# Kernel tuning notes

Measured on AMD Instinct MI355X. Metric: run time of the kernel, lower is better.

Reference implementation:

```python
import jax, jax.numpy as jnp
import numpy as np

EPS = 1e-12
B, S, H, NH = 4, 2048, 512, 8
DH = H // NH

def layernorm(x, g, b):
    mu = jnp.mean(x, axis=-1, keepdims=True)
    var = jnp.mean((x - mu) ** 2, axis=-1, keepdims=True)
    return (x - mu) * jax.lax.rsqrt(var + EPS) * g + b

def setup_inputs() -> dict:
    key = jax.random.key(0)
    ks = jax.random.split(key, 12)
    s = 0.02
    return {
        "hidden_states": jax.random.normal(ks[0], (B, S, H), dtype=jnp.float32),
        "attention_mask": jnp.zeros((B, 1, 1, S), dtype=jnp.float32),
        "ln1_g": jnp.ones((H,), jnp.float32), "ln1_b": jnp.zeros((H,), jnp.float32),
        "wq": jax.random.normal(ks[1], (H, H), jnp.float32) * s, "bq": jnp.zeros((H,), jnp.float32),
        "wk": jax.random.normal(ks[2], (H, H), jnp.float32) * s, "bk": jnp.zeros((H,), jnp.float32),
        "wv": jax.random.normal(ks[3], (H, H), jnp.float32) * s, "bv": jnp.zeros((H,), jnp.float32),
        "wo": jax.random.normal(ks[4], (H, H), jnp.float32) * s, "bo": jnp.zeros((H,), jnp.float32),
        "ln2_g": jnp.ones((H,), jnp.float32), "ln2_b": jnp.zeros((H,), jnp.float32),
    }

def _heads(x):  # [B,S,H] -> [B,NH,S,DH]
    return x.reshape(B, S, NH, DH).transpose(0, 2, 1, 3)

def reference(hidden_states, attention_mask, ln1_g, ln1_b, wq, bq, wk, bk, wv, bv, wo, bo, ln2_g, ln2_b):
    h = layernorm(hidden_states, ln1_g, ln1_b)  # Pre-LN
    q = _heads(h @ wq.T + bq)
    k = _heads(h @ wk.T + bk)
    v = _heads(h @ wv.T + bv)
    scores = jnp.einsum("bhqd,bhkd->bhqk", q, k) / jnp.sqrt(jnp.float32(DH))
    scores = scores + attention_mask  # additive BERT mask
    probs = jax.nn.softmax(scores, axis=-1)
    ctx = jnp.einsum("bhqk,bhkd->bhqd", probs, v)
    ctx = ctx.transpose(0, 2, 1, 3).reshape(B, S, H)
    # BertSelfOutput: LN(dense(ctx) + residual), residual is the LN'd hidden per module code
    out = layernorm(ctx @ wo.T + bo + h, ln2_g, ln2_b)
    return out
```

## Files before the change

kernel.cpp:

```cpp
#include <hip/hip_runtime.h>

typedef __bf16 bf16;
typedef __bf16 bf16x2 __attribute__((ext_vector_type(2)));
typedef __bf16 bf16x4 __attribute__((ext_vector_type(4)));
typedef __bf16 bf16x8 __attribute__((ext_vector_type(8)));
typedef float f32x4 __attribute__((ext_vector_type(4)));

typedef __attribute__((address_space(1))) const void g_void;
typedef __attribute__((address_space(3))) void l_void;

constexpr int Bsz = 4, S = 2048, H = 512, NH = 8, DH = 64;
constexpr int M = Bsz * S;
constexpr int K = H;
constexpr int WELEM = H * H;
constexpr float LOG2E  = 1.44269504f;
constexpr float QSCALE = 0.125f * LOG2E;

__global__ __launch_bounds__(256) void convert_w(
    const float* __restrict__ w0, const float* __restrict__ w1,
    const float* __restrict__ w2, const float* __restrict__ w3,
    bf16* __restrict__ dst) {
    int y = blockIdx.y;
    const float* src = (y == 0) ? w0 : (y == 1) ? w1 : (y == 2) ? w2 : w3;
    bf16* d = dst + (size_t)y * WELEM;
    int i = (blockIdx.x * 256 + threadIdx.x) * 4;
    float4 v = *(const float4*)(src + i);
    bf16x4 o;
    o.x = (bf16)v.x; o.y = (bf16)v.y; o.z = (bf16)v.z; o.w = (bf16)v.w;
    *(bf16x4*)(d + i) = o;
}

__global__ __launch_bounds__(256) void scale_mask(
    const float* __restrict__ m, float* __restrict__ out) {
    int i = blockIdx.x * 256 + threadIdx.x;
    out[i] = m[i] * LOG2E;
}

__global__ __launch_bounds__(256) void ln_f32_bf16(
    const float* __restrict__ x, const float* __restrict__ g,
    const float* __restrict__ b, bf16* __restrict__ y) {
    int row = blockIdx.x;
    int t = threadIdx.x;
    float2 xv = *(const float2*)(x + (size_t)row * H + t * 2);
    float v0 = xv.x, v1 = xv.y;
    float s = v0 + v1, s2 = v0 * v0 + v1 * v1;
    for (int off = 1; off < 64; off <<= 1) {
        s  += __shfl_xor(s,  off, 64);
        s2 += __shfl_xor(s2, off, 64);
    }
    __shared__ float red[8];
    int wid = t >> 6;
    if ((t & 63) == 0) { red[wid * 2] = s; red[wid * 2 + 1] = s2; }
    __syncthreads();
    s  = red[0] + red[2] + red[4] + red[6];
    s2 = red[1] + red[3] + red[5] + red[7];
    float mu  = s * (1.0f / H);
    float var = s2 * (1.0f / H) - mu * mu;
    float inv = rsqrtf(var + 1e-12f);
    float2 gv = *(const float2*)(g + t * 2);
    float2 bv = *(const float2*)(b + t * 2);
    bf16x2 out;
    out.x = (bf16)((v0 - mu) * inv * gv.x + bv.x);
    out.y = (bf16)((v1 - mu) * inv * gv.y + bv.y);
    *(bf16x2*)(y + (size_t)row * H + t * 2) = out;
}

__global__ __launch_bounds__(256) void ln_bf16_f32(
    const bf16* __restrict__ x, const float* __restrict__ g,
    const float* __restrict__ b, float* __restrict__ y) {
    int row = blockIdx.x;
    int t = threadIdx.x;
    bf16x2 xv = *(const bf16x2*)(x + (size_t)row * H + t * 2);
    float v0 = (float)xv.x, v1 = (float)xv.y;
    float s = v0 + v1, s2 = v0 * v0 + v1 * v1;
    for (int off = 1; off < 64; off <<= 1) {
        s  += __shfl_xor(s,  off, 64);
        s2 += __shfl_xor(s2, off, 64);
    }
    __shared__ float red[8];
    int wid = t >> 6;
    if ((t & 63) == 0) { red[wid * 2] = s; red[wid * 2 + 1] = s2; }
    __syncthreads();
    s  = red[0] + red[2] + red[4] + red[6];
    s2 = red[1] + red[3] + red[5] + red[7];
    float mu  = s * (1.0f / H);
    float var = s2 * (1.0f / H) - mu * mu;
    float inv = rsqrtf(var + 1e-12f);
    float2 gv = *(const float2*)(g + t * 2);
    float2 bv = *(const float2*)(b + t * 2);
    float2 out;
    out.x = (v0 - mu) * inv * gv.x + bv.x;
    out.y = (v1 - mu) * inv * gv.y + bv.y;
    *(float2*)(y + (size_t)row * H + t * 2) = out;
}

__device__ inline void gemm128_mainloop(const bf16* __restrict__ A,
                                        const bf16* __restrict__ W,
                                        int bm, int bn,
                                        bf16* As, bf16* Bs, f32x4 acc[4][4]) {
    int t = threadIdx.x;
    int lane = t & 63, wid = t >> 6;
    int quad = lane >> 4, n = lane & 15;
    int wm = wid & 1, wn = wid >> 1;
    int sw = (n & 7) * 8;
    int srow = lane >> 3;
    int scol = (lane & 7) * 8;
    for (int kt = 0; kt < K; kt += 64) {
        __syncthreads();
        #pragma unroll
        for (int i = 0; i < 4; i++) {
            int chunk = wid * 4 + i;
            int row = chunk * 8 + srow;
            int csrc = scol ^ ((row & 7) * 8);
            __builtin_amdgcn_global_load_lds(
                (g_void*)&A[(size_t)(bm + row) * K + kt + csrc],
                (l_void*)&As[chunk * 512], 16, 0, 0);
            __builtin_amdgcn_global_load_lds(
                (g_void*)&W[(size_t)(bn + row) * K + kt + csrc],
                (l_void*)&Bs[chunk * 512], 16, 0, 0);
        }
        __syncthreads();
        #pragma unroll
        for (int half = 0; half < 2; half++) {
            bf16x8 af[4], bf[4];
            #pragma unroll
            for (int mi = 0; mi < 4; mi++) {
                int c = (half * 32 + quad * 8) ^ sw;
                af[mi] = *(const bf16x8*)&As[(wm * 64 + mi * 16 + n) * 64 + c];
                bf[mi] = *(const bf16x8*)&Bs[(wn * 64 + mi * 16 + n) * 64 + c];
            }
            #pragma unroll
            for (int mi = 0; mi < 4; mi++)
                #pragma unroll
                for (int ni = 0; ni < 4; ni++)
                    acc[mi][ni] = __builtin_amdgcn_mfma_f32_16x16x32_bf16(
                        af[mi], bf[ni], acc[mi][ni], 0, 0, 0);
        }
    }
}

__global__ __launch_bounds__(256) void gemm_qkv(
    const bf16* __restrict__ h, const bf16* __restrict__ wb,
    const float* __restrict__ bq, const float* __restrict__ bk,
    const float* __restrict__ bv,
    bf16* __restrict__ qd, bf16* __restrict__ kd, bf16* __restrict__ vtd) {
    __shared__ alignas(16) bf16 As[128 * 64];
    __shared__ alignas(16) bf16 Bs[128 * 64];
    int bm = blockIdx.x * 128, bn = blockIdx.y * 128, z = blockIdx.z;
    const bf16* W = wb + (size_t)z * WELEM;
    const float* bias = (z == 0) ? bq : (z == 1) ? bk : bv;
    f32x4 acc[4][4];
    for (int mi = 0; mi < 4; mi++)
        for (int ni = 0; ni < 4; ni++)
            for (int r = 0; r < 4; r++) acc[mi][ni][r] = 0.0f;
    gemm128_mainloop(h, W, bm, bn, As, Bs, acc);
    int lane = threadIdx.x & 63, wid = threadIdx.x >> 6;
    int quad = lane >> 4, n = lane & 15;
    int wm = wid & 1, wn = wid >> 1;
    for (int mi = 0; mi < 4; mi++)
        for (int ni = 0; ni < 4; ni++)
            for (int r = 0; r < 4; r++) {
                int i = bm + wm * 64 + mi * 16 + quad * 4 + r;
                int j = bn + wn * 64 + ni * 16 + n;
                float val = acc[mi][ni][r] + bias[j];
                if (z == 0) val *= QSCALE;
                int b = i >> 11, srow = i & (S - 1);
                int nh = j >> 6, d = j & (DH - 1);
                if (z < 2) {
                    bf16* dst = (z == 0) ? qd : kd;
                    dst[(((size_t)(b * NH + nh)) * S + srow) * DH + d] = (bf16)val;
                } else {
                    vtd[(((size_t)(b * NH + nh)) * DH + d) * S + srow] = (bf16)val;
                }
            }
}

__global__ __launch_bounds__(256) void gemm_out(
    const bf16* __restrict__ ctx, const bf16* __restrict__ wo,
    const float* __restrict__ bo, const bf16* __restrict__ resid,
    bf16* __restrict__ dst) {
    __shared__ alignas(16) bf16 As[128 * 64];
    __shared__ alignas(16) bf16 Bs[128 * 64];
    int bm = blockIdx.x * 128, bn = blockIdx.y * 128;
    f32x4 acc[4][4];
    for (int mi = 0; mi < 4; mi++)
        for (int ni = 0; ni < 4; ni++)
            for (int r = 0; r < 4; r++) acc[mi][ni][r] = 0.0f;
    gemm128_mainloop(ctx, wo, bm, bn, As, Bs, acc);
    int lane = threadIdx.x & 63, wid = threadIdx.x >> 6;
    int quad = lane >> 4, n = lane & 15;
    int wm = wid & 1, wn = wid >> 1;
    for (int mi = 0; mi < 4; mi++)
        for (int ni = 0; ni < 4; ni++)
            for (int r = 0; r < 4; r++) {
                int i = bm + wm * 64 + mi * 16 + quad * 4 + r;
                int j = bn + wn * 64 + ni * 16 + n;
                float val = acc[mi][ni][r] + bo[j]
                          + (float)resid[(size_t)i * H + j];
                dst[(size_t)i * H + j] = (bf16)val;
            }
}

constexpr int LDP9 = 72;

#if __has_builtin(__builtin_amdgcn_exp2f)
#define EXP2(x) __builtin_amdgcn_exp2f(x)
#else
#define EXP2(x) exp2f(x)
#endif

__global__ __launch_bounds__(512, 4) void attn_kernel(
    const bf16* __restrict__ q, const bf16* __restrict__ k,
    const bf16* __restrict__ vt, const float* __restrict__ mask2,
    bf16* __restrict__ ctx) {
    int bh = blockIdx.y;
    int b = bh >> 3, nh = bh & 7;
    int t = threadIdx.x, wid = t >> 6, lane = t & 63;
    int quad = lane >> 4, n = lane & 15;
    int qg = wid >> 1, kh = wid & 1;
    int qbase = blockIdx.x * 128 + qg * 32;
    int kO = kh * 64;

    const bf16* Qp = q  + (size_t)bh * S * DH;
    const bf16* Kp = k  + (size_t)bh * S * DH;
    const bf16* Vt = vt + (size_t)bh * DH * S;
    const float* mrow = mask2 + (size_t)b * S;

    __shared__ alignas(16) bf16 smem[34816];
    bf16* Ks = smem;
    bf16* Vs = smem + 8192;
    bf16* Pw = smem + 16384 + wid * (32 * LDP9);

    int sw = (n & 7) * 8;

    bf16x8 qf[2][2];
    #pragma unroll
    for (int qt = 0; qt < 2; qt++)
        #pragma unroll
        for (int hh = 0; hh < 2; hh++)
            qf[qt][hh] = *(const bf16x8*)
                &Qp[(size_t)(qbase + qt * 16 + n) * DH + hh * 32 + quad * 8];

    f32x4 O[2][4];
    #pragma unroll
    for (int qt = 0; qt < 2; qt++)
        for (int i = 0; i < 4; i++)
            for (int r = 0; r < 4; r++) O[qt][i][r] = 0.0f;
    float l_run[2] = {0.0f, 0.0f};

    for (int kb = 0; kb < S; kb += 128) {
        __syncthreads();
        #pragma unroll
        for (int i = 0; i < 2; i++) {
            int c = t + i * 512;
            {
                int row = c >> 3, part = c & 7;
                int csrc = (part * 8) ^ ((row & 7) * 8);
                __builtin_amdgcn_global_load_lds(
                    (g_void*)&Kp[(size_t)(kb + row) * DH + csrc],
                    (l_void*)&Ks[c * 8], 16, 0, 0);
            }
            {
                int row = c >> 4, part = c & 15;
                int csrc = (part * 8) ^ ((row & 7) * 8);
                __builtin_amdgcn_global_load_lds(
                    (g_void*)&Vt[(size_t)row * S + kb + csrc],
                    (l_void*)&Vs[c * 8], 16, 0, 0);
            }
        }
        __syncthreads();

        #pragma unroll
        for (int kt = 0; kt < 4; kt++) {
            const bf16* kr = &Ks[(kO + kt * 16 + n) * 64];
            bf16x8 ka = *(const bf16x8*)&kr[(quad * 8) ^ sw];
            bf16x8 kc = *(const bf16x8*)&kr[(32 + quad * 8) ^ sw];
            float4 mk = *(const float4*)&mrow[kb + kO + kt * 16 + quad * 4];
            #pragma unroll
            for (int qt = 0; qt < 2; qt++) {
                f32x4 s;
                for (int r = 0; r < 4; r++) s[r] = 0.0f;
                s = __builtin_amdgcn_mfma_f32_16x16x32_bf16(ka, qf[qt][0], s, 0, 0, 0);
                s = __builtin_amdgcn_mfma_f32_16x16x32_bf16(kc, qf[qt][1], s, 0, 0, 0);
                float p0 = EXP2(s[0] + mk.x);
                float p1 = EXP2(s[1] + mk.y);
                float p2 = EXP2(s[2] + mk.z);
                float p3 = EXP2(s[3] + mk.w);
                l_run[qt] += (p0 + p1) + (p2 + p3);
                bf16x4 w;
                w[0] = (bf16)p0; w[1] = (bf16)p1; w[2] = (bf16)p2; w[3] = (bf16)p3;
                *(bf16x4*)&Pw[(qt * 16 + n) * LDP9 + kt * 16 + quad * 4] = w;
            }
        }

        __builtin_amdgcn_s_setprio(1);
        #pragma unroll
        for (int ks = 0; ks < 2; ks++)
            #pragma unroll
            for (int qt = 0; qt < 2; qt++) {
                bf16x8 pf = *(const bf16x8*)
                    &Pw[(qt * 16 + n) * LDP9 + ks * 32 + quad * 8];
                #pragma unroll
                for (int dt = 0; dt < 4; dt++) {
                    bf16x8 vf = *(const bf16x8*)
                        &Vs[(dt * 16 + n) * 128 + ((kO + ks * 32 + quad * 8) ^ sw)];
                    O[qt][dt] = __builtin_amdgcn_mfma_f32_16x16x32_bf16(
                        vf, pf, O[qt][dt], 0, 0, 0);
                }
            }
        __builtin_amdgcn_s_setprio(0);
    }

    float* Ob = (float*)smem;
    float* Lb = Ob + 4 * 32 * 68;
    __syncthreads();
    if (kh) {
        #pragma unroll
        for (int qt = 0; qt < 2; qt++) {
            #pragma unroll
            for (int dt = 0; dt < 4; dt++)
                *(f32x4*)&Ob[(qg * 32 + qt * 16 + n) * 68 + dt * 16 + quad * 4]
                    = O[qt][dt];
            Lb[(qg * 2 + qt) * 64 + lane] = l_run[qt];
        }
    }
    __syncthreads();
    if (!kh) {
        #pragma unroll
        for (int qt = 0; qt < 2; qt++) {
            float l = l_run[qt] + Lb[(qg * 2 + qt) * 64 + lane];
            l += __shfl_xor(l, 16, 64);
            l += __shfl_xor(l, 32, 64);
            float linv = 1.0f / l;
            int srow = qbase + qt * 16 + n;
            #pragma unroll
            for (int dt = 0; dt < 4; dt++) {
                f32x4 po = *(const f32x4*)
                    &Ob[(qg * 32 + qt * 16 + n) * 68 + dt * 16 + quad * 4];
                bf16x4 o4;
                for (int r = 0; r < 4; r++)
                    o4[r] = (bf16)((O[qt][dt][r] + po[r]) * linv);
                int col = nh * 64 + dt * 16 + quad * 4;
                *(bf16x4*)&ctx[((size_t)(b * S + srow)) * H + col] = o4;
            }
        }
    }
}

extern "C" void kernel_launch(void* const* d_in, const int* in_sizes, int n_in,
                              void* d_out, int out_size, void* d_ws, size_t ws_size,
                              hipStream_t stream) {
    const float* hidden = (const float*)d_in[0];
    const float* mask   = (const float*)d_in[1];
    const float* ln1_g  = (const float*)d_in[2];
    const float* ln1_b  = (const float*)d_in[3];
    const float* wq = (const float*)d_in[4],  *bq = (const float*)d_in[5];
    const float* wk = (const float*)d_in[6],  *bk = (const float*)d_in[7];
    const float* wv = (const float*)d_in[8],  *bv = (const float*)d_in[9];
    const float* wo = (const float*)d_in[10], *bo = (const float*)d_in[11];
    const float* ln2_g = (const float*)d_in[12];
    const float* ln2_b = (const float*)d_in[13];

    const size_t T = (size_t)M * H;
    bf16* wb  = (bf16*)d_ws;
    bf16* h   = wb  + (size_t)4 * WELEM;
    bf16* qd  = h   + T;
    bf16* kd  = qd  + T;
    bf16* vtd = kd  + T;
    bf16* ctx = vtd + T;
    float* mask2 = (float*)(ctx + T);
    bf16* tmp = qd;

    convert_w<<<dim3(WELEM / 1024, 4), 256, 0, stream>>>(wq, wk, wv, wo, wb);
    scale_mask<<<Bsz * S / 256, 256, 0, stream>>>(mask, mask2);
    ln_f32_bf16<<<M, 256, 0, stream>>>(hidden, ln1_g, ln1_b, h);
    gemm_qkv<<<dim3(M / 128, H / 128, 3), 256, 0, stream>>>(
        h, wb, bq, bk, bv, qd, kd, vtd);
    attn_kernel<<<dim3(S / 128, Bsz * NH), 512, 0, stream>>>(qd, kd, vtd, mask2, ctx);
    gemm_out<<<dim3(M / 128, H / 128), 256, 0, stream>>>(
        ctx, wb + (size_t)3 * WELEM, bo, h, tmp);
    ln_bf16_f32<<<M, 256, 0, stream>>>(tmp, ln2_g, ln2_b, (float*)d_out);
}
```

Baseline: 202.1 us.

## Fuse prep kernels and stage V-transpose through shared memory for coalesced stores

Merges the weight conversion, mask scaling and first LayerNorm into a single launch, with block ranges selecting the task, so two kernel launches go away. In the QKV GEMM, the V-transpose epilogue now writes the tile into padded shared memory and then stores 16-byte vectors along the sequence dimension, replacing the scattered 2-byte strided global writes. This costs an extra shared-memory buffer and two barriers in the V blocks.

```diff
diff --git a/kernel.cpp b/kernel.cpp
--- a/kernel.cpp
+++ b/kernel.cpp
@@ -16,53 +16,53 @@
 constexpr float LOG2E  = 1.44269504f;
 constexpr float QSCALE = 0.125f * LOG2E;
 
-__global__ __launch_bounds__(256) void convert_w(
+__global__ __launch_bounds__(256) void prep(
+    const float* __restrict__ hidden, const float* __restrict__ ln1_g,
+    const float* __restrict__ ln1_b,
     const float* __restrict__ w0, const float* __restrict__ w1,
     const float* __restrict__ w2, const float* __restrict__ w3,
-    bf16* __restrict__ dst) {
-    int y = blockIdx.y;
-    const float* src = (y == 0) ? w0 : (y == 1) ? w1 : (y == 2) ? w2 : w3;
-    bf16* d = dst + (size_t)y * WELEM;
-    int i = (blockIdx.x * 256 + threadIdx.x) * 4;
-    float4 v = *(const float4*)(src + i);
-    bf16x4 o;
-    o.x = (bf16)v.x; o.y = (bf16)v.y; o.z = (bf16)v.z; o.w = (bf16)v.w;
-    *(bf16x4*)(d + i) = o;
-}
-
-__global__ __launch_bounds__(256) void scale_mask(
-    const float* __restrict__ m, float* __restrict__ out) {
-    int i = blockIdx.x * 256 + threadIdx.x;
-    out[i] = m[i] * LOG2E;
-}
-
-__global__ __launch_bounds__(256) void ln_f32_bf16(
-    const float* __restrict__ x, const float* __restrict__ g,
-    const float* __restrict__ b, bf16* __restrict__ y) {
-    int row = blockIdx.x;
+    const float* __restrict__ mask,
+    bf16* __restrict__ h, bf16* __restrict__ wb, float* __restrict__ mask2) {
+    int bx = blockIdx.x;
     int t = threadIdx.x;
-    float2 xv = *(const float2*)(x + (size_t)row * H + t * 2);
-    float v0 = xv.x, v1 = xv.y;
-    float s = v0 + v1, s2 = v0 * v0 + v1 * v1;
-    for (int off = 1; off < 64; off <<= 1) {
-        s  += __shfl_xor(s,  off, 64);
-        s2 += __shfl_xor(s2, off, 64);
-    }
-    __shared__ float red[8];
-    int wid = t >> 6;
-    if ((t & 63) == 0) { red[wid * 2] = s; red[wid * 2 + 1] = s2; }
-    __syncthreads();
-    s  = red[0] + red[2] + red[4] + red[6];
-    s2 = red[1] + red[3] + red[5] + red[7];
-    float mu  = s * (1.0f / H);
-    float var = s2 * (1.0f / H) - mu * mu;
-    float inv = rsqrtf(var + 1e-12f);
-    float2 gv = *(const float2*)(g + t * 2);
-    float2 bv = *(const float2*)(b + t * 2);
-    bf16x2 out;
-    out.x = (bf16)((v0 - mu) * inv * gv.x + bv.x);
-    out.y = (bf16)((v1 - mu) * inv * gv.y + bv.y);
-    *(bf16x2*)(y + (size_t)row * H + t * 2) = out;
+    if (bx < M) {
+        int row = bx;
+        float2 xv = *(const float2*)(hidden + (size_t)row * H + t * 2);
+        float v0 = xv.x, v1 = xv.y;
+        float s = v0 + v1, s2 = v0 * v0 + v1 * v1;
+        for (int off = 1; off < 64; off <<= 1) {
+            s  += __shfl_xor(s,  off, 64);
+            s2 += __shfl_xor(s2, off, 64);
+        }
+        __shared__ float red[8];
+        int wid = t >> 6;
+        if ((t & 63) == 0) { red[wid * 2] = s; red[wid * 2 + 1] = s2; }
+        __syncthreads();
+        s  = red[0] + red[2] + red[4] + red[6];
+        s2 = red[1] + red[3] + red[5] + red[7];
+        float mu  = s * (1.0f / H);
+        float var = s2 * (1.0f / H) - mu * mu;
+        float inv = rsqrtf(var + 1e-12f);
+        float2 gv = *(const float2*)(ln1_g + t * 2);
+        float2 bv = *(const float2*)(ln1_b + t * 2);
+        bf16x2 out;
+        out.x = (bf16)((v0 - mu) * inv * gv.x + bv.x);
+        out.y = (bf16)((v1 - mu) * inv * gv.y + bv.y);
+        *(bf16x2*)(h + (size_t)row * H + t * 2) = out;
+    } else if (bx < M + 1024) {
+        int idx = bx - M;
+        int y = idx >> 8, xx = idx & 255;
+        const float* src = (y == 0) ? w0 : (y == 1) ? w1 : (y == 2) ? w2 : w3;
+        bf16* d = wb + (size_t)y * WELEM;
+        int i = (xx * 256 + t) * 4;
+        float4 v = *(const float4*)(src + i);
+        bf16x4 o;
+        o.x = (bf16)v.x; o.y = (bf16)v.y; o.z = (bf16)v.z; o.w = (bf16)v.w;
+        *(bf16x4*)(d + i) = o;
+    } else {
+        int i = (bx - M - 1024) * 256 + t;
+        mask2[i] = mask[i] * LOG2E;
+    }
 }
 
 __global__ __launch_bounds__(256) void ln_bf16_f32(
@@ -144,8 +144,9 @@
     const float* __restrict__ bq, const float* __restrict__ bk,
     const float* __restrict__ bv,
     bf16* __restrict__ qd, bf16* __restrict__ kd, bf16* __restrict__ vtd) {
-    __shared__ alignas(16) bf16 As[128 * 64];
-    __shared__ alignas(16) bf16 Bs[128 * 64];
+    __shared__ alignas(16) bf16 smem[17408];
+    bf16* As = smem;
+    bf16* Bs = smem + 8192;
     int bm = blockIdx.x * 128, bn = blockIdx.y * 128, z = blockIdx.z;
     const bf16* W = wb + (size_t)z * WELEM;
     const float* bias = (z == 0) ? bq : (z == 1) ? bk : bv;
@@ -154,25 +155,47 @@
         for (int ni = 0; ni < 4; ni++)
             for (int r = 0; r < 4; r++) acc[mi][ni][r] = 0.0f;
     gemm128_mainloop(h, W, bm, bn, As, Bs, acc);
-    int lane = threadIdx.x & 63, wid = threadIdx.x >> 6;
+    int t = threadIdx.x;
+    int lane = t & 63, wid = t >> 6;
     int quad = lane >> 4, n = lane & 15;
     int wm = wid & 1, wn = wid >> 1;
-    for (int mi = 0; mi < 4; mi++)
-        for (int ni = 0; ni < 4; ni++)
-            for (int r = 0; r < 4; r++) {
-                int i = bm + wm * 64 + mi * 16 + quad * 4 + r;
-                int j = bn + wn * 64 + ni * 16 + n;
-                float val = acc[mi][ni][r] + bias[j];
-                if (z == 0) val *= QSCALE;
-                int b = i >> 11, srow = i & (S - 1);
-                int nh = j >> 6, d = j & (DH - 1);
-                if (z < 2) {
-                    bf16* dst = (z == 0) ? qd : kd;
+    if (z < 2) {
+        bf16* dst = (z == 0) ? qd : kd;
+        for (int mi = 0; mi < 4; mi++)
+            for (int ni = 0; ni < 4; ni++)
+                for (int r = 0; r < 4; r++) {
+                    int i = bm + wm * 64 + mi * 16 + quad * 4 + r;
+                    int j = bn + wn * 64 + ni * 16 + n;
+                    float val = acc[mi][ni][r] + bias[j];
+                    if (z == 0) val *= QSCALE;
+                    int b = i >> 11, srow = i & (S - 1);
+                    int nh = j >> 6, d = j & (DH - 1);
                     dst[(((size_t)(b * NH + nh)) * S + srow) * DH + d] = (bf16)val;
-                } else {
-                    vtd[(((size_t)(b * NH + nh)) * DH + d) * S + srow] = (bf16)val;
                 }
-            }
+    } else {
+        __syncthreads();
+        bf16* T = smem;
+        for (int mi = 0; mi < 4; mi++)
+            for (int ni = 0; ni < 4; ni++)
+                for (int r = 0; r < 4; r++) {
+                    int il = wm * 64 + mi * 16 + quad * 4 + r;
+                    int jl = wn * 64 + ni * 16 + n;
+                    float val = acc[mi][ni][r] + bias[bn + jl];
+                    T[jl * 136 + il] = (bf16)val;
+                }
+        __syncthreads();
+        int b = bm >> 11, srow0 = bm & (S - 1);
+        int c16 = t & 15;
+        #pragma unroll
+        for (int p = 0; p < 8; p++) {
+            int jl = (t >> 4) + p * 16;
+            int j = bn + jl;
+            int nh = j >> 6, d = j & (DH - 1);
+            bf16x8 v = *(const bf16x8*)&T[jl * 136 + c16 * 8];
+            *(bf16x8*)&vtd[(((size_t)(b * NH + nh)) * DH + d) * S
+                           + srow0 + c16 * 8] = v;
+        }
+    }
 }
 
 __global__ __launch_bounds__(256) void gemm_out(
@@ -371,9 +394,8 @@
     float* mask2 = (float*)(ctx + T);
     bf16* tmp = qd;
 
-    convert_w<<<dim3(WELEM / 1024, 4), 256, 0, stream>>>(wq, wk, wv, wo, wb);
-    scale_mask<<<Bsz * S / 256, 256, 0, stream>>>(mask, mask2);
-    ln_f32_bf16<<<M, 256, 0, stream>>>(hidden, ln1_g, ln1_b, h);
+    prep<<<M + 1024 + 32, 256, 0, stream>>>(
+        hidden, ln1_g, ln1_b, wq, wk, wv, wo, mask, h, wb, mask2);
     gemm_qkv<<<dim3(M / 128, H / 128, 3), 256, 0, stream>>>(
         h, wb, bq, bk, bv, qd, kd, vtd);
     attn_kernel<<<dim3(S / 128, Bsz * NH), 512, 0, stream>>>(qd, kd, vtd, mask2, ctx);
```

New measurement: 193.0 us. 1.05x faster.
